# Optimization experiments

Measured on AMD Instinct MI355X. Metric: run time of the kernel, lower is better.

The kernel has to match this reference:

```python
import jax, jax.numpy as jnp
import numpy as np

N = 100000      # nodes
E = 3200000     # edges (avg degree 32)
D_IN, H, D_OUT = 512, 16, 64


def setup_inputs() -> dict:
    key = jax.random.key(0)
    k = jax.random.split(key, 7)
    x = jax.random.normal(k[0], (N, D_IN), dtype=jnp.float32)
    edge_index = jax.random.randint(k[1], (2, E), 0, N, dtype=jnp.int64)
    edge_weight = jax.random.uniform(k[2], (E,), dtype=jnp.float32)
    W1 = jax.random.normal(k[3], (D_IN, H), dtype=jnp.float32) * (1.0 / np.sqrt(D_IN))
    b1 = jnp.zeros((H,), dtype=jnp.float32)
    W2 = jax.random.normal(k[4], (H, D_OUT), dtype=jnp.float32) * (1.0 / np.sqrt(H))
    b2 = jnp.zeros((D_OUT,), dtype=jnp.float32)
    return {"x": x, "edge_index": edge_index, "edge_weight": edge_weight,
            "W1": W1, "b1": b1, "W2": W2, "b2": b2}


def _gcn_conv(x, edge_index, edge_weight, W, b):
    """PyG GCNConv (normalize=True, add self-loops): D^-1/2 (A+I) D^-1/2 (x W) + b."""
    n = x.shape[0]
    src, dst = edge_index[0], edge_index[1]
    loop = jnp.arange(n, dtype=src.dtype)
    row = jnp.concatenate([src, loop])            # message source
    col = jnp.concatenate([dst, loop])            # aggregation target
    w = jnp.concatenate([edge_weight, jnp.ones((n,), x.dtype)])
    deg = jax.ops.segment_sum(w, col, num_segments=n)
    dinv = jnp.where(deg > 0, jax.lax.rsqrt(deg), 0.0)
    norm = dinv[row] * w * dinv[col]              # [E+N]
    h = x @ W                                     # linear before propagate (PyG order)
    msg = h[row] * norm[:, None]                  # gather + scale, [E+N, d_out]
    out = jax.ops.segment_sum(msg, col, num_segments=n)  # scatter-add
    return out + b


def reference(x, edge_index, edge_weight, W1, b1, W2, b2):
    h = jax.nn.relu(_gcn_conv(x, edge_index, edge_weight, W1, b1))
    # F.dropout(training=self.training): identity in eval mode
    return _gcn_conv(h, edge_index, edge_weight, W2, b2)
```

## Files before the change

kernel.cpp:

```cpp
#include <hip/hip_runtime.h>
#include <hip/hip_fp16.h>


constexpr int BKT_BITS = 8;
constexpr int BKT = 1 << BKT_BITS;
constexpr int EPB = 8192;

__device__ __forceinline__ unsigned long long nt_load_u64(const void* p) {
  return __builtin_nontemporal_load((const unsigned long long*)p);
}

__global__ __launch_bounds__(256) void k_pre(
    const float* __restrict__ x, const float* __restrict__ W1,
    float* __restrict__ h1pre, int n,
    const int* __restrict__ dst, int* __restrict__ hist, int ne, int nb,
    int xw1b) {
  __shared__ float W1t[16 * 512];
  if ((int)blockIdx.x >= xw1b) {
    int* sh = (int*)W1t;
    int hb = blockIdx.x - xw1b;
    for (int i = threadIdx.x; i < nb; i += 256) sh[i] = 0;
    __syncthreads();
    int base = hb * EPB;
    int end = min(base + EPB, ne);
    for (int e = base + threadIdx.x; e < end; e += 256)
      atomicAdd(&sh[dst[e] >> BKT_BITS], 1);
    __syncthreads();
    for (int i = threadIdx.x; i < nb; i += 256) hist[hb * nb + i] = sh[i];
    return;
  }
  {
#pragma unroll
    for (int i = 0; i < 32; ++i) {
      int idx = threadIdx.x + i * 256;
      int k = idx >> 4, j = idx & 15;
      W1t[j * 512 + k] = W1[idx];
    }
  }
  __syncthreads();
  int gtid = blockIdx.x * 256 + threadIdx.x;
  int rp = gtid >> 2, q = gtid & 3;
  int r0 = rp * 2;
  if (r0 >= n) return;
  int r1 = r0 + 1;
  bool has1 = (r1 < n);
  const float4* x4 = (const float4*)x;
  const float4* W1t4 = (const float4*)W1t;
  float acc0[16], acc1[16];
#pragma unroll
  for (int j = 0; j < 16; ++j) { acc0[j] = 0.f; acc1[j] = 0.f; }
  long rb0 = (long)r0 * 128 + q;
  long rb1 = (long)r1 * 128 + q;
  for (int m = 0; m < 32; ++m) {
    float4 a = x4[rb0 + m * 4];
    float4 b = has1 ? x4[rb1 + m * 4] : make_float4(0.f, 0.f, 0.f, 0.f);
    int p = q + m * 4;
#pragma unroll
    for (int j = 0; j < 16; ++j) {
      float4 w = W1t4[j * 128 + p];
      acc0[j] = fmaf(a.x, w.x, acc0[j]);
      acc0[j] = fmaf(a.y, w.y, acc0[j]);
      acc0[j] = fmaf(a.z, w.z, acc0[j]);
      acc0[j] = fmaf(a.w, w.w, acc0[j]);
      acc1[j] = fmaf(b.x, w.x, acc1[j]);
      acc1[j] = fmaf(b.y, w.y, acc1[j]);
      acc1[j] = fmaf(b.z, w.z, acc1[j]);
      acc1[j] = fmaf(b.w, w.w, acc1[j]);
    }
  }
#pragma unroll
  for (int j = 0; j < 16; ++j) {
    acc0[j] += __shfl_xor(acc0[j], 1);
    acc0[j] += __shfl_xor(acc0[j], 2);
    acc1[j] += __shfl_xor(acc1[j], 1);
    acc1[j] += __shfl_xor(acc1[j], 2);
  }
  if (q == 0) {
    float4* o4 = (float4*)h1pre;
#pragma unroll
    for (int j4 = 0; j4 < 4; ++j4) {
      o4[(long)r0 * 4 + j4] =
          make_float4(acc0[4 * j4], acc0[4 * j4 + 1], acc0[4 * j4 + 2], acc0[4 * j4 + 3]);
      if (has1)
        o4[(long)r1 * 4 + j4] =
            make_float4(acc1[4 * j4], acc1[4 * j4 + 1], acc1[4 * j4 + 2], acc1[4 * j4 + 3]);
    }
  }
}

__global__ __launch_bounds__(256) void k_colscan(
    const int* __restrict__ hist, int* __restrict__ basep,
    int* __restrict__ colsum, int nblk, int nb) {
  __shared__ int sh[256];
  __shared__ int carry_s;
  int k = blockIdx.x;
  int t = threadIdx.x;
  if (t == 0) carry_s = 0;
  __syncthreads();
  for (int c0 = 0; c0 < nblk; c0 += 256) {
    int b = c0 + t;
    int v = (b < nblk) ? hist[b * nb + k] : 0;
    sh[t] = v;
    __syncthreads();
    for (int d = 1; d < 256; d <<= 1) {
      int u = (t >= d) ? sh[t - d] : 0;
      __syncthreads();
      sh[t] += u;
      __syncthreads();
    }
    if (b < nblk) basep[b * nb + k] = carry_s + sh[t] - v;
    __syncthreads();
    if (t == 0) carry_s += sh[255];
    __syncthreads();
  }
  if (t == 0) colsum[k] = carry_s;
}

__global__ __launch_bounds__(256) void k_scanb(
    const int* __restrict__ colsum, int* __restrict__ bstart, int nb) {
  __shared__ int sh[256];
  __shared__ int carry_s;
  int t = threadIdx.x;
  if (t == 0) carry_s = 0;
  __syncthreads();
  for (int c0 = 0; c0 < nb; c0 += 256) {
    int k = c0 + t;
    int v = (k < nb) ? colsum[k] : 0;
    sh[t] = v;
    __syncthreads();
    for (int d = 1; d < 256; d <<= 1) {
      int u = (t >= d) ? sh[t - d] : 0;
      __syncthreads();
      sh[t] += u;
      __syncthreads();
    }
    if (k < nb) bstart[k] = carry_s + sh[t] - v;
    __syncthreads();
    if (t == 0) carry_s += sh[255];
    __syncthreads();
  }
  if (t == 0) bstart[nb] = carry_s;
}

__global__ __launch_bounds__(256) void k_binfill(
    const int* __restrict__ ei, const float* __restrict__ ew,
    const int* __restrict__ basep, const int* __restrict__ bstart,
    uint2* __restrict__ recs, int ne, int nb) {
  extern __shared__ int cur[];
  for (int i = threadIdx.x; i < nb; i += 256)
    cur[i] = basep[blockIdx.x * nb + i] + bstart[i];
  __syncthreads();
  int bs = blockIdx.x * EPB;
  int end = min(bs + EPB, ne);
  for (int e = bs + threadIdx.x; e < end; e += 256) {
    int s = ei[e];
    int d = ei[ne + e];
    float w = ew[e];
    int bkt = d >> BKT_BITS;
    int pos = atomicAdd(&cur[bkt], 1);
    recs[pos] = make_uint2((unsigned)s | ((unsigned)(d & (BKT - 1)) << 20),
                           __float_as_uint(w));
  }
}

__global__ __launch_bounds__(256) void k_csr(
    const uint2* __restrict__ recs, const int* __restrict__ bstart,
    uint2* __restrict__ csr, int* __restrict__ rowptr,
    float* __restrict__ dinv, const float* __restrict__ h1pre,
    __half2* __restrict__ hp16, int n, int ne) {
  __shared__ float sdeg[BKT];
  __shared__ int soff[BKT];
  __shared__ int scur[BKT];
  int t = threadIdx.x;
  sdeg[t] = 0.f;
  soff[t] = 0;
  __syncthreads();
  int k = blockIdx.x;
  int s0 = bstart[k], s1 = bstart[k + 1];
  for (int e = s0 + t; e < s1; e += 256) {
    uint2 r = recs[e];
    int dl = (r.x >> 20) & (BKT - 1);
    atomicAdd(&soff[dl], 1);
    atomicAdd(&sdeg[dl], __uint_as_float(r.y));
  }
  __syncthreads();
  int v = soff[t];
  for (int d = 1; d < BKT; d <<= 1) {
    int u = (t >= d) ? soff[t - d] : 0;
    __syncthreads();
    soff[t] += u;
    __syncthreads();
  }
  int excl = soff[t] - v;
  scur[t] = excl;
  int node = (k << BKT_BITS) + t;
  float dvv = 0.f;
  if (node < n) {
    dvv = 1.0f / sqrtf(sdeg[t] + 1.0f);
    rowptr[node] = s0 + excl;
    dinv[node] = dvv;
  }
  sdeg[t] = dvv;
  if (k == 0 && t == 0) rowptr[n] = ne;
  __syncthreads();
  for (int e = s0 + t; e < s1; e += 256) {
    uint2 r = recs[e];
    int dl = (r.x >> 20) & (BKT - 1);
    int pos = s0 + atomicAdd(&scur[dl], 1);
    csr[pos] = make_uint2(r.x & 0xFFFFF, r.y);
  }
  int nbase = k << BKT_BITS;
  int nn = min(n - nbase, BKT);
  if (nn > 0) {
    const float2* hf2 = (const float2*)h1pre + (long)nbase * 8;
    __half2* hp2 = hp16 + (long)nbase * 8;
    int lim2 = nn * 8;
    for (int i = t; i < lim2; i += 256) {
      float dv2 = sdeg[i >> 3];
      float2 hv = hf2[i];
      hp2[i] = __floats2half2_rn(hv.x * dv2, hv.y * dv2);
    }
  }
}

template <int MODE>
__global__ __launch_bounds__(256) void k_agg(
    const __half2* __restrict__ hin2, const uint2* __restrict__ csr,
    const int* __restrict__ rowptr, const float* __restrict__ dinv,
    const float* __restrict__ bias, const float* __restrict__ W2,
    void* __restrict__ outv, int n) {
  __shared__ float W2s[MODE == 2 ? 16 * 64 : 1];
  __shared__ float accs[MODE == 2 ? 64 * 16 : 1];
  if (MODE == 2) {
#pragma unroll
    for (int s = 0; s < 4; ++s) W2s[threadIdx.x + s * 256] = W2[threadIdx.x + s * 256];
  }
  int gtid = blockIdx.x * 256 + threadIdx.x;
  int node = gtid >> 2, q = gtid & 3;
  bool valid = node < n;
  float4 acc = make_float4(0.f, 0.f, 0.f, 0.f);
  float dv = 0.f;
  if (valid) {
    dv = dinv[node];
    int hb = (node << 3) + (q << 1);
    {
      float2 f0 = __half22float2(hin2[hb]);
      float2 f1 = __half22float2(hin2[hb + 1]);
      acc = make_float4(f0.x, f0.y, f1.x, f1.y);
    }
    int e = rowptr[node], e1 = rowptr[node + 1];
    for (; e + 7 < e1; e += 8) {
      unsigned long long rv[8];
#pragma unroll
      for (int u = 0; u < 8; ++u) rv[u] = nt_load_u64(&csr[e + u]);
      float2 g0[8], g1[8];
      float wv[8];
#pragma unroll
      for (int u = 0; u < 8; ++u) {
        int src = (int)(unsigned)rv[u];
        wv[u] = __uint_as_float((unsigned)(rv[u] >> 32));
        int b = (src << 3) + (q << 1);
        g0[u] = __half22float2(hin2[b]);
        g1[u] = __half22float2(hin2[b + 1]);
      }
#pragma unroll
      for (int u = 0; u < 8; ++u) {
        acc.x = fmaf(wv[u], g0[u].x, acc.x);
        acc.y = fmaf(wv[u], g0[u].y, acc.y);
        acc.z = fmaf(wv[u], g1[u].x, acc.z);
        acc.w = fmaf(wv[u], g1[u].y, acc.w);
      }
    }
    for (; e < e1; ++e) {
      unsigned long long rv = nt_load_u64(&csr[e]);
      int src = (int)(unsigned)rv;
      float w = __uint_as_float((unsigned)(rv >> 32));
      int b = (src << 3) + (q << 1);
      float2 f0 = __half22float2(hin2[b]);
      float2 f1 = __half22float2(hin2[b + 1]);
      acc.x = fmaf(w, f0.x, acc.x);
      acc.y = fmaf(w, f0.y, acc.y);
      acc.z = fmaf(w, f1.x, acc.z);
      acc.w = fmaf(w, f1.y, acc.w);
    }
    acc.x *= dv; acc.y *= dv; acc.z *= dv; acc.w *= dv;
  }
  if (MODE == 1) {
    if (valid) {
      float4 b = ((const float4*)bias)[q];
      __half2* o2 = (__half2*)outv;
      int hb = (node << 3) + (q << 1);
      o2[hb] = __floats2half2_rn(dv * fmaxf(acc.x + b.x, 0.f),
                                 dv * fmaxf(acc.y + b.y, 0.f));
      o2[hb + 1] = __floats2half2_rn(dv * fmaxf(acc.z + b.z, 0.f),
                                     dv * fmaxf(acc.w + b.w, 0.f));
    }
    return;
  }
  ((float4*)accs)[threadIdx.x] = acc;
  __syncthreads();
  const float4* W2s4 = (const float4*)W2s;
  float* out = (float*)outv;
#pragma unroll
  for (int it = 0; it < 4; ++it) {
    int nl = it * 16 + (threadIdx.x >> 4);
    int o4 = threadIdx.x & 15;
    int node2 = blockIdx.x * 64 + nl;
    if (node2 < n) {
      float4 v = ((const float4*)bias)[o4];
#pragma unroll
      for (int jj = 0; jj < 16; ++jj) {
        float a = accs[nl * 16 + jj];
        float4 w = W2s4[jj * 16 + o4];
        v.x = fmaf(a, w.x, v.x);
        v.y = fmaf(a, w.y, v.y);
        v.z = fmaf(a, w.z, v.z);
        v.w = fmaf(a, w.w, v.w);
      }
      ((float4*)out)[(long)node2 * 16 + o4] = v;
    }
  }
}

extern "C" void kernel_launch(void* const* d_in, const int* in_sizes, int n_in,
                              void* d_out, int out_size, void* d_ws, size_t ws_size,
                              hipStream_t stream) {
  const float* x  = (const float*)d_in[0];
  const int*   ei = (const int*)d_in[1];
  const float* ew = (const float*)d_in[2];
  const float* W1 = (const float*)d_in[3];
  const float* b1 = (const float*)d_in[4];
  const float* W2 = (const float*)d_in[5];
  const float* b2 = (const float*)d_in[6];
  float* out = (float*)d_out;
  int n  = in_sizes[0] / 512;
  int ne = in_sizes[1] / 2;

  int nb   = (n + BKT - 1) >> BKT_BITS;
  int nblk = (ne + EPB - 1) / EPB;

  char* ws = (char*)d_ws;
  size_t off = 0;
  auto alloc = [&](size_t bytes) {
    size_t r = off;
    off += (bytes + 255) & ~(size_t)255;
    return r;
  };
  float*   dinv   = (float*)  (ws + alloc((size_t)n * 4));
  float*   h1pre  = (float*)  (ws + alloc((size_t)n * 16 * 4));
  __half2* hp16   = (__half2*)(ws + alloc((size_t)n * 16 * 2));
  __half2* h1p16  = (__half2*)(ws + alloc((size_t)n * 16 * 2));
  uint2*   recs   = (uint2*)  (ws + alloc((size_t)ne * 8));
  uint2*   csr    = (uint2*)  (ws + alloc((size_t)ne * 8));
  int*     rowptr = (int*)    (ws + alloc((size_t)(n + 1) * 4));
  int*     hist   = (int*)    (ws + alloc((size_t)nblk * nb * 4));
  int*     basep  = (int*)    (ws + alloc((size_t)nblk * nb * 4));
  int*     colsum = (int*)    (ws + alloc((size_t)nb * 4));
  int*     bstart = (int*)    (ws + alloc((size_t)(nb + 1) * 4));
  (void)ws_size; (void)n_in; (void)out_size;

  int nrp = (n + 1) / 2;
  int xw1b = (nrp * 4 + 255) / 256;
  k_pre<<<xw1b + nblk, 256, 0, stream>>>(x, W1, h1pre, n, ei + ne, hist, ne, nb, xw1b);

  k_colscan<<<nb, 256, 0, stream>>>(hist, basep, colsum, nblk, nb);
  k_scanb<<<1, 256, 0, stream>>>(colsum, bstart, nb);
  size_t shb = (size_t)nb * 4;
  k_binfill<<<nblk, 256, shb, stream>>>(ei, ew, basep, bstart, recs, ne, nb);
  k_csr<<<nb, 256, 0, stream>>>(recs, bstart, csr, rowptr, dinv, h1pre, hp16, n, ne);

  int gN4 = (n * 4 + 255) / 256;
  k_agg<1><<<gN4, 256, 0, stream>>>(hp16, csr, rowptr, dinv, b1, nullptr, h1p16, n);
  k_agg<2><<<gN4, 256, 0, stream>>>(h1p16, csr, rowptr, dinv, b2, W2, out, n);
}
```

Before: 270.2 us.

## Use MFMA fp16 for x@W1, fuse scan kernels, simplify aggregation loads

```diff
diff --git a/kernel.cpp b/kernel.cpp
--- a/kernel.cpp
+++ b/kernel.cpp
@@ -6,18 +6,17 @@
 constexpr int BKT = 1 << BKT_BITS;
 constexpr int EPB = 8192;
 
-__device__ __forceinline__ unsigned long long nt_load_u64(const void* p) {
-  return __builtin_nontemporal_load((const unsigned long long*)p);
-}
+typedef _Float16 f16x8 __attribute__((ext_vector_type(8)));
+typedef float f32x4 __attribute__((ext_vector_type(4)));
 
 __global__ __launch_bounds__(256) void k_pre(
     const float* __restrict__ x, const float* __restrict__ W1,
     float* __restrict__ h1pre, int n,
     const int* __restrict__ dst, int* __restrict__ hist, int ne, int nb,
-    int xw1b) {
-  __shared__ float W1t[16 * 512];
+    int xw1b, int* __restrict__ donecnt) {
+  if (blockIdx.x == 0 && threadIdx.x == 0) *donecnt = 0;
   if ((int)blockIdx.x >= xw1b) {
-    int* sh = (int*)W1t;
+    __shared__ int sh[512];
     int hb = blockIdx.x - xw1b;
     for (int i = threadIdx.x; i < nb; i += 256) sh[i] = 0;
     __syncthreads();
@@ -29,70 +28,53 @@
     for (int i = threadIdx.x; i < nb; i += 256) hist[hb * nb + i] = sh[i];
     return;
   }
-  {
-#pragma unroll
-    for (int i = 0; i < 32; ++i) {
-      int idx = threadIdx.x + i * 256;
-      int k = idx >> 4, j = idx & 15;
-      W1t[j * 512 + k] = W1[idx];
-    }
-  }
-  __syncthreads();
-  int gtid = blockIdx.x * 256 + threadIdx.x;
-  int rp = gtid >> 2, q = gtid & 3;
-  int r0 = rp * 2;
-  if (r0 >= n) return;
-  int r1 = r0 + 1;
-  bool has1 = (r1 < n);
+  int lane = threadIdx.x & 63;
+  int j16 = lane & 15;
+  int kh = lane >> 4;
+  f16x8 wf[16];
+#pragma unroll
+  for (int kb = 0; kb < 16; ++kb) {
+    f16x8 w;
+#pragma unroll
+    for (int i = 0; i < 8; ++i)
+      w[i] = (_Float16)W1[(kb * 32 + kh * 8 + i) * 16 + j16];
+    wf[kb] = w;
+  }
+  int tiles = (n + 15) >> 4;
+  int wid = (blockIdx.x * 256 + threadIdx.x) >> 6;
+  if (wid >= tiles) return;
+  int tile16 = wid << 4;
+  int arow = tile16 + j16;
+  if (arow >= n) arow = n - 1;
   const float4* x4 = (const float4*)x;
-  const float4* W1t4 = (const float4*)W1t;
-  float acc0[16], acc1[16];
-#pragma unroll
-  for (int j = 0; j < 16; ++j) { acc0[j] = 0.f; acc1[j] = 0.f; }
-  long rb0 = (long)r0 * 128 + q;
-  long rb1 = (long)r1 * 128 + q;
-  for (int m = 0; m < 32; ++m) {
-    float4 a = x4[rb0 + m * 4];
-    float4 b = has1 ? x4[rb1 + m * 4] : make_float4(0.f, 0.f, 0.f, 0.f);
-    int p = q + m * 4;
-#pragma unroll
-    for (int j = 0; j < 16; ++j) {
-      float4 w = W1t4[j * 128 + p];
-      acc0[j] = fmaf(a.x, w.x, acc0[j]);
-      acc0[j] = fmaf(a.y, w.y, acc0[j]);
-      acc0[j] = fmaf(a.z, w.z, acc0[j]);
-      acc0[j] = fmaf(a.w, w.w, acc0[j]);
-      acc1[j] = fmaf(b.x, w.x, acc1[j]);
-      acc1[j] = fmaf(b.y, w.y, acc1[j]);
-      acc1[j] = fmaf(b.z, w.z, acc1[j]);
-      acc1[j] = fmaf(b.w, w.w, acc1[j]);
-    }
-  }
-#pragma unroll
-  for (int j = 0; j < 16; ++j) {
-    acc0[j] += __shfl_xor(acc0[j], 1);
-    acc0[j] += __shfl_xor(acc0[j], 2);
-    acc1[j] += __shfl_xor(acc1[j], 1);
-    acc1[j] += __shfl_xor(acc1[j], 2);
-  }
-  if (q == 0) {
-    float4* o4 = (float4*)h1pre;
-#pragma unroll
-    for (int j4 = 0; j4 < 4; ++j4) {
-      o4[(long)r0 * 4 + j4] =
-          make_float4(acc0[4 * j4], acc0[4 * j4 + 1], acc0[4 * j4 + 2], acc0[4 * j4 + 3]);
-      if (has1)
-        o4[(long)r1 * 4 + j4] =
-            make_float4(acc1[4 * j4], acc1[4 * j4 + 1], acc1[4 * j4 + 2], acc1[4 * j4 + 3]);
-    }
+  long rb = (long)arow * 128 + kh * 2;
+  f32x4 acc = {0.f, 0.f, 0.f, 0.f};
+#pragma unroll
+  for (int kb = 0; kb < 16; ++kb) {
+    float4 a0 = x4[rb + kb * 8];
+    float4 a1 = x4[rb + kb * 8 + 1];
+    f16x8 af;
+    af[0] = (_Float16)a0.x; af[1] = (_Float16)a0.y;
+    af[2] = (_Float16)a0.z; af[3] = (_Float16)a0.w;
+    af[4] = (_Float16)a1.x; af[5] = (_Float16)a1.y;
+    af[6] = (_Float16)a1.z; af[7] = (_Float16)a1.w;
+    acc = __builtin_amdgcn_mfma_f32_16x16x32_f16(af, wf[kb], acc, 0, 0, 0);
+  }
+  int i0 = tile16 + kh * 4;
+#pragma unroll
+  for (int r = 0; r < 4; ++r) {
+    int row = i0 + r;
+    if (row < n) h1pre[(long)row * 16 + j16] = acc[r];
   }
 }
 
 __global__ __launch_bounds__(256) void k_colscan(
     const int* __restrict__ hist, int* __restrict__ basep,
-    int* __restrict__ colsum, int nblk, int nb) {
+    int* __restrict__ colsum, int* __restrict__ bstart,
+    int* __restrict__ donecnt, int nblk, int nb) {
   __shared__ int sh[256];
   __shared__ int carry_s;
+  __shared__ int is_last;
   int k = blockIdx.x;
   int t = threadIdx.x;
   if (t == 0) carry_s = 0;
@@ -113,19 +95,20 @@
     if (t == 0) carry_s += sh[255];
     __syncthreads();
   }
-  if (t == 0) colsum[k] = carry_s;
-}
-
-__global__ __launch_bounds__(256) void k_scanb(
-    const int* __restrict__ colsum, int* __restrict__ bstart, int nb) {
-  __shared__ int sh[256];
-  __shared__ int carry_s;
-  int t = threadIdx.x;
+  if (t == 0) atomicExch(&colsum[k], carry_s);
+  __threadfence();
+  if (t == 0) {
+    int ticket = atomicAdd(donecnt, 1);
+    is_last = (ticket == (int)gridDim.x - 1);
+  }
+  __syncthreads();
+  if (!is_last) return;
+  __threadfence();
   if (t == 0) carry_s = 0;
   __syncthreads();
   for (int c0 = 0; c0 < nb; c0 += 256) {
-    int k = c0 + t;
-    int v = (k < nb) ? colsum[k] : 0;
+    int kk = c0 + t;
+    int v = (kk < nb) ? atomicAdd(&colsum[kk], 0) : 0;
     sh[t] = v;
     __syncthreads();
     for (int d = 1; d < 256; d <<= 1) {
@@ -134,7 +117,7 @@
       sh[t] += u;
       __syncthreads();
     }
-    if (k < nb) bstart[k] = carry_s + sh[t] - v;
+    if (kk < nb) bstart[kk] = carry_s + sh[t] - v;
     __syncthreads();
     if (t == 0) carry_s += sh[255];
     __syncthreads();
@@ -225,7 +208,7 @@
 
 template <int MODE>
 __global__ __launch_bounds__(256) void k_agg(
-    const __half2* __restrict__ hin2, const uint2* __restrict__ csr,
+    const uint2* __restrict__ hin8, const uint2* __restrict__ csr,
     const int* __restrict__ rowptr, const float* __restrict__ dinv,
     const float* __restrict__ bias, const float* __restrict__ W2,
     void* __restrict__ outv, int n) {
@@ -242,42 +225,44 @@
   float dv = 0.f;
   if (valid) {
     dv = dinv[node];
-    int hb = (node << 3) + (q << 1);
     {
-      float2 f0 = __half22float2(hin2[hb]);
-      float2 f1 = __half22float2(hin2[hb + 1]);
+      uint2 u = hin8[node * 4 + q];
+      float2 f0 = __half22float2(*(const __half2*)&u.x);
+      float2 f1 = __half22float2(*(const __half2*)&u.y);
       acc = make_float4(f0.x, f0.y, f1.x, f1.y);
     }
     int e = rowptr[node], e1 = rowptr[node + 1];
-    for (; e + 7 < e1; e += 8) {
-      unsigned long long rv[8];
-#pragma unroll
-      for (int u = 0; u < 8; ++u) rv[u] = nt_load_u64(&csr[e + u]);
-      float2 g0[8], g1[8];
-      float wv[8];
-#pragma unroll
-      for (int u = 0; u < 8; ++u) {
-        int src = (int)(unsigned)rv[u];
-        wv[u] = __uint_as_float((unsigned)(rv[u] >> 32));
-        int b = (src << 3) + (q << 1);
-        g0[u] = __half22float2(hin2[b]);
-        g1[u] = __half22float2(hin2[b + 1]);
-      }
-#pragma unroll
-      for (int u = 0; u < 8; ++u) {
-        acc.x = fmaf(wv[u], g0[u].x, acc.x);
-        acc.y = fmaf(wv[u], g0[u].y, acc.y);
-        acc.z = fmaf(wv[u], g1[u].x, acc.z);
-        acc.w = fmaf(wv[u], g1[u].y, acc.w);
-      }
+    for (; e + 3 < e1; e += 4) {
+      uint2 r0 = csr[e], r1 = csr[e + 1], r2 = csr[e + 2], r3 = csr[e + 3];
+      uint2 g0 = hin8[r0.x * 4 + q];
+      uint2 g1 = hin8[r1.x * 4 + q];
+      uint2 g2 = hin8[r2.x * 4 + q];
+      uint2 g3 = hin8[r3.x * 4 + q];
+      float w0 = __uint_as_float(r0.y), w1 = __uint_as_float(r1.y);
+      float w2 = __uint_as_float(r2.y), w3 = __uint_as_float(r3.y);
+      float2 a0 = __half22float2(*(const __half2*)&g0.x);
+      float2 b0 = __half22float2(*(const __half2*)&g0.y);
+      float2 a1 = __half22float2(*(const __half2*)&g1.x);
+      float2 b1v = __half22float2(*(const __half2*)&g1.y);
+      float2 a2 = __half22float2(*(const __half2*)&g2.x);
+      float2 b2v = __half22float2(*(const __half2*)&g2.y);
+      float2 a3 = __half22float2(*(const __half2*)&g3.x);
+      float2 b3 = __half22float2(*(const __half2*)&g3.y);
+      acc.x = fmaf(w0, a0.x, acc.x); acc.y = fmaf(w0, a0.y, acc.y);
+      acc.z = fmaf(w0, b0.x, acc.z); acc.w = fmaf(w0, b0.y, acc.w);
+      acc.x = fmaf(w1, a1.x, acc.x); acc.y = fmaf(w1, a1.y, acc.y);
+      acc.z = fmaf(w1, b1v.x, acc.z); acc.w = fmaf(w1, b1v.y, acc.w);
+      acc.x = fmaf(w2, a2.x, acc.x); acc.y = fmaf(w2, a2.y, acc.y);
+      acc.z = fmaf(w2, b2v.x, acc.z); acc.w = fmaf(w2, b2v.y, acc.w);
+      acc.x = fmaf(w3, a3.x, acc.x); acc.y = fmaf(w3, a3.y, acc.y);
+      acc.z = fmaf(w3, b3.x, acc.z); acc.w = fmaf(w3, b3.y, acc.w);
     }
     for (; e < e1; ++e) {
-      unsigned long long rv = nt_load_u64(&csr[e]);
-      int src = (int)(unsigned)rv;
-      float w = __uint_as_float((unsigned)(rv >> 32));
-      int b = (src << 3) + (q << 1);
-      float2 f0 = __half22float2(hin2[b]);
-      float2 f1 = __half22float2(hin2[b + 1]);
+      uint2 r = csr[e];
+      uint2 g = hin8[r.x * 4 + q];
+      float w = __uint_as_float(r.y);
+      float2 f0 = __half22float2(*(const __half2*)&g.x);
+      float2 f1 = __half22float2(*(const __half2*)&g.y);
       acc.x = fmaf(w, f0.x, acc.x);
       acc.y = fmaf(w, f0.y, acc.y);
       acc.z = fmaf(w, f1.x, acc.z);
@@ -288,12 +273,14 @@
   if (MODE == 1) {
     if (valid) {
       float4 b = ((const float4*)bias)[q];
-      __half2* o2 = (__half2*)outv;
-      int hb = (node << 3) + (q << 1);
-      o2[hb] = __floats2half2_rn(dv * fmaxf(acc.x + b.x, 0.f),
-                                 dv * fmaxf(acc.y + b.y, 0.f));
-      o2[hb + 1] = __floats2half2_rn(dv * fmaxf(acc.z + b.z, 0.f),
+      __half2 lo = __floats2half2_rn(dv * fmaxf(acc.x + b.x, 0.f),
+                                     dv * fmaxf(acc.y + b.y, 0.f));
+      __half2 hi = __floats2half2_rn(dv * fmaxf(acc.z + b.z, 0.f),
                                      dv * fmaxf(acc.w + b.w, 0.f));
+      uint2 o;
+      o.x = *(const unsigned*)&lo;
+      o.y = *(const unsigned*)&hi;
+      ((uint2*)outv)[node * 4 + q] = o;
     }
     return;
   }
@@ -346,30 +333,33 @@
     off += (bytes + 255) & ~(size_t)255;
     return r;
   };
-  float*   dinv   = (float*)  (ws + alloc((size_t)n * 4));
-  float*   h1pre  = (float*)  (ws + alloc((size_t)n * 16 * 4));
-  __half2* hp16   = (__half2*)(ws + alloc((size_t)n * 16 * 2));
-  __half2* h1p16  = (__half2*)(ws + alloc((size_t)n * 16 * 2));
-  uint2*   recs   = (uint2*)  (ws + alloc((size_t)ne * 8));
-  uint2*   csr    = (uint2*)  (ws + alloc((size_t)ne * 8));
-  int*     rowptr = (int*)    (ws + alloc((size_t)(n + 1) * 4));
-  int*     hist   = (int*)    (ws + alloc((size_t)nblk * nb * 4));
-  int*     basep  = (int*)    (ws + alloc((size_t)nblk * nb * 4));
-  int*     colsum = (int*)    (ws + alloc((size_t)nb * 4));
-  int*     bstart = (int*)    (ws + alloc((size_t)(nb + 1) * 4));
+  float*   dinv    = (float*)  (ws + alloc((size_t)n * 4));
+  float*   h1pre   = (float*)  (ws + alloc((size_t)n * 16 * 4));
+  __half2* hp16    = (__half2*)(ws + alloc((size_t)n * 16 * 2));
+  __half2* h1p16   = (__half2*)(ws + alloc((size_t)n * 16 * 2));
+  uint2*   recs    = (uint2*)  (ws + alloc((size_t)ne * 8));
+  uint2*   csr     = (uint2*)  (ws + alloc((size_t)ne * 8));
+  int*     rowptr  = (int*)    (ws + alloc((size_t)(n + 1) * 4));
+  int*     hist    = (int*)    (ws + alloc((size_t)nblk * nb * 4));
+  int*     basep   = (int*)    (ws + alloc((size_t)nblk * nb * 4));
+  int*     colsum  = (int*)    (ws + alloc((size_t)nb * 4));
+  int*     bstart  = (int*)    (ws + alloc((size_t)(nb + 1) * 4));
+  int*     donecnt = (int*)    (ws + alloc(4));
   (void)ws_size; (void)n_in; (void)out_size;
 
-  int nrp = (n + 1) / 2;
-  int xw1b = (nrp * 4 + 255) / 256;
-  k_pre<<<xw1b + nblk, 256, 0, stream>>>(x, W1, h1pre, n, ei + ne, hist, ne, nb, xw1b);
-
-  k_colscan<<<nb, 256, 0, stream>>>(hist, basep, colsum, nblk, nb);
-  k_scanb<<<1, 256, 0, stream>>>(colsum, bstart, nb);
+  int tiles = (n + 15) / 16;
+  int xw1b = (tiles + 3) / 4;
+  k_pre<<<xw1b + nblk, 256, 0, stream>>>(x, W1, h1pre, n, ei + ne, hist, ne, nb,
+                                         xw1b, donecnt);
+
+  k_colscan<<<nb, 256, 0, stream>>>(hist, basep, colsum, bstart, donecnt, nblk, nb);
   size_t shb = (size_t)nb * 4;
   k_binfill<<<nblk, 256, shb, stream>>>(ei, ew, basep, bstart, recs, ne, nb);
   k_csr<<<nb, 256, 0, stream>>>(recs, bstart, csr, rowptr, dinv, h1pre, hp16, n, ne);
 
   int gN4 = (n * 4 + 255) / 256;
-  k_agg<1><<<gN4, 256, 0, stream>>>(hp16, csr, rowptr, dinv, b1, nullptr, h1p16, n);
-  k_agg<2><<<gN4, 256, 0, stream>>>(h1p16, csr, rowptr, dinv, b2, W2, out, n);
-}
+  k_agg<1><<<gN4, 256, 0, stream>>>((const uint2*)hp16, csr, rowptr, dinv, b1,
+                                    nullptr, h1p16, n);
+  k_agg<2><<<gN4, 256, 0, stream>>>((const uint2*)h1p16, csr, rowptr, dinv, b2,
+                                    W2, out, n);
+}
```

After: 281.3 us. 1.04x slower.
